# Kernel tuning notes

Measured on AMD Instinct MI355X. Metric: run time of the kernel, lower is better.

## Reference

```python
import jax, jax.numpy as jnp
import numpy as np

N_E = 1024
E_DIM = 64
BETA = 0.25


def setup_inputs() -> dict:
    key = jax.random.key(0)
    k1, k2 = jax.random.split(key)
    z = jax.random.normal(k1, (16, E_DIM, 64, 64), dtype=jnp.float32)
    # torch init: uniform(-1/n_e, 1/n_e)
    emb_w = jax.random.uniform(k2, (N_E, E_DIM), dtype=jnp.float32,
                               minval=-1.0 / N_E, maxval=1.0 / N_E)
    return {"z": z, "emb_w": emb_w}


def reference(z, emb_w):
    bt, ch, h, w = z.shape
    # (B, C, H, W) -> (B, H, W, C) -> (N, e_dim)
    z_perm = jnp.transpose(z, (0, 2, 3, 1))
    z_flat = z_perm.reshape(-1, ch)  # (N, e_dim)

    # squared euclidean distances: (N, n_e)
    distances = (jnp.sum(z_flat ** 2, axis=1, keepdims=True)
                 + jnp.sum(emb_w ** 2, axis=1)
                 - 2.0 * jnp.matmul(z_flat, emb_w.T))
    min_idx = jnp.argmin(distances, axis=1)  # (N,)

    min_encodings = jax.nn.one_hot(min_idx, N_E, dtype=z.dtype)  # (N, n_e)

    # gather codebook vectors (same math as one_hot @ emb_w)
    z_q = emb_w[min_idx].reshape(bt, h, w, ch)
    z_q = jnp.transpose(z_q, (0, 3, 1, 2))  # (B, C, H, W)

    commitment_loss = BETA * jnp.mean((jax.lax.stop_gradient(z_q) - z) ** 2)
    loss = commitment_loss

    # straight-through estimator
    z_q_st = z + jax.lax.stop_gradient(z_q - z)

    avg_probs = jnp.mean(min_encodings, axis=0)
    perplexity = jnp.exp(-jnp.sum(avg_probs * jnp.log(avg_probs + 1e-10)))

    min_encoding_indices = min_idx.reshape(bt, h, w)
    return loss, z_q_st, perplexity, min_encodings, min_encoding_indices
```

## Files before the change

### kernel.cpp

```cpp
#include <hip/hip_runtime.h>
#include <math.h>

#define NPOS   65536
#define NE     1024
#define EDIM   64
#define HW     4096
#define BETA   0.25

#define OUT_LOSS 0LL
#define OUT_ZQ   1LL
#define OUT_PERP 4194305LL
#define OUT_ENC  4194306LL
#define OUT_IDX  71303170LL

__device__ __forceinline__ float pairwise_sum_sq64(const float v[64]) {
#pragma clang fp contract(off)
    float r[8];
#pragma unroll
    for (int k = 0; k < 8; ++k) r[k] = v[k] * v[k];
#pragma unroll
    for (int i = 8; i < 64; i += 8) {
#pragma unroll
        for (int k = 0; k < 8; ++k) {
            float s = v[i + k] * v[i + k];
            r[k] = r[k] + s;
        }
    }
    return ((r[0] + r[1]) + (r[2] + r[3])) + ((r[4] + r[5]) + (r[6] + r[7]));
}

__global__ void vq_prep(const float* __restrict__ emb, float* __restrict__ enorm,
                        int* __restrict__ counts, double* __restrict__ lacc) {
    int t = blockIdx.x * 256 + threadIdx.x;
    if (t < NE) {
        float v[64];
#pragma unroll
        for (int c = 0; c < 64; ++c) v[c] = emb[t * 64 + c];
        enorm[t] = pairwise_sum_sq64(v);
        counts[t] = 0;
    }
    if (t == 0) *lacc = 0.0;
}

__global__ __launch_bounds__(256, 4)
void vq_main(const float* __restrict__ z, const float* __restrict__ emb,
             const float* __restrict__ enorm, int* __restrict__ counts,
             double* __restrict__ lacc, float* __restrict__ out) {
    __shared__ float dl[256];
    __shared__ int   il[256];
    __shared__ int   fidx[64];

    const int tid = threadIdx.x;
    const int l   = tid & 63;
    const int w   = tid >> 6;
    const int n0  = blockIdx.x * 64;
    const int b   = n0 >> 12;
    const int hw0 = n0 & 4095;
    const long long zoff = (long long)b * (64LL * HW) + hw0 + l;

    float zv[64];
#pragma unroll
    for (int c = 0; c < 64; ++c) zv[c] = z[zoff + (long long)c * HW];

    const float szn = pairwise_sum_sq64(zv);

    const int jbase = __builtin_amdgcn_readfirstlane(w * 256);

    float best = 3.4e38f;
    int   bi   = jbase;
#pragma unroll 2
    for (int jj = 0; jj < 256; ++jj) {
        const int j = jbase + jj;
        const float* __restrict__ erow = emb + j * 64;
        float acc = 0.0f;
#pragma unroll
        for (int c = 0; c < 64; ++c) acc = fmaf(zv[c], erow[c], acc);
        float dj = (szn + enorm[j]) - 2.0f * acc;
        if (dj < best) { best = dj; bi = j; }
    }
    dl[tid] = best;
    il[tid] = bi;
    __syncthreads();

    if (w == 0) {
        float bd = dl[l];
        int   bx = il[l];
#pragma unroll
        for (int ww = 1; ww < 4; ++ww) {
            float dw = dl[ww * 64 + l];
            int   iw = il[ww * 64 + l];
            if (dw < bd) { bd = dw; bx = iw; }
        }
        fidx[l] = bx;
        atomicAdd(&counts[bx], 1);
        out[OUT_IDX + n0 + l] = (float)bx;
    }
    __syncthreads();

    {
        float2* __restrict__ enc = (float2*)(out + OUT_ENC);
        const int c0 = tid * 2;
        const int c1 = (tid + 256) * 2;
        for (int r = 0; r < 64; ++r) {
            const int ir = fidx[r];
            const long long rowb = (long long)(n0 + r) * 512;
            float2 v0, v1;
            v0.x = (ir == c0)     ? 1.0f : 0.0f;
            v0.y = (ir == c0 + 1) ? 1.0f : 0.0f;
            v1.x = (ir == c1)     ? 1.0f : 0.0f;
            v1.y = (ir == c1 + 1) ? 1.0f : 0.0f;
            enc[rowb + tid]       = v0;
            enc[rowb + 256 + tid] = v1;
        }
    }

    const int myidx = fidx[l];
    double acc = 0.0;
#pragma unroll
    for (int k = 0; k < 16; ++k) {
        const int c = w * 16 + k;
        const float zc = z[zoff + (long long)c * HW];
        const float ec = emb[myidx * 64 + c];
        const float t  = __fsub_rn(ec, zc);
        const float o  = __fadd_rn(zc, t);
        out[OUT_ZQ + (long long)b * (64LL * HW) + (long long)c * HW + hw0 + l] = o;
        const float s = __fmul_rn(t, t);
        acc += (double)s;
    }
#pragma unroll
    for (int off = 32; off > 0; off >>= 1) acc += __shfl_down(acc, off);
    if (l == 0) atomicAdd(lacc, acc);
}

__global__ void vq_finalize(const int* __restrict__ counts,
                            const double* __restrict__ lacc,
                            float* __restrict__ out) {
    __shared__ float red[1024];
    const int t = threadIdx.x;
    const float p = (float)counts[t] * (1.0f / 65536.0f);
    const float term = p * logf(p + 1e-10f);
    red[t] = term;
    __syncthreads();
    for (int s = 512; s > 0; s >>= 1) {
        if (t < s) red[t] += red[t + s];
        __syncthreads();
    }
    if (t == 0) {
        out[OUT_PERP] = expf(-red[0]);
        out[OUT_LOSS] = (float)(BETA * (*lacc / 4194304.0));
    }
}

extern "C" void kernel_launch(void* const* d_in, const int* in_sizes, int n_in,
                              void* d_out, int out_size, void* d_ws, size_t ws_size,
                              hipStream_t stream) {
    const float* z   = (const float*)d_in[0];
    const float* emb = (const float*)d_in[1];
    float* out = (float*)d_out;

    double* lacc  = (double*)d_ws;
    int*    cnts  = (int*)((char*)d_ws + 16);
    float*  enorm = (float*)((char*)d_ws + 16 + NE * sizeof(int));

    vq_prep<<<4, 256, 0, stream>>>(emb, enorm, cnts, lacc);
    vq_main<<<1024, 256, 0, stream>>>(z, emb, enorm, cnts, lacc, out);
    vq_finalize<<<1, 1024, 0, stream>>>(cnts, lacc, out);
}
```

Measured before the change: 215.0 us.

## Transpose codebook and compute distances in 32-code register tiles

The prep kernel now writes a transposed copy of the codebook. The main kernel computes 32 code distances at once, streaming z one channel at a time instead of holding all 64 z values in registers. This aims to cut register pressure and increase reuse of each z load across many codes, at the cost of reloading z from memory for every 32-code tile. Offsets are also narrowed to 32-bit integers.

After: 197.1 us. 8.3% less time.

```diff
diff --git a/kernel.cpp b/kernel.cpp
--- a/kernel.cpp
+++ b/kernel.cpp
@@ -30,13 +30,16 @@
 }
 
 __global__ void vq_prep(const float* __restrict__ emb, float* __restrict__ enorm,
-                        int* __restrict__ counts, double* __restrict__ lacc) {
+                        float* __restrict__ embT, int* __restrict__ counts,
+                        double* __restrict__ lacc) {
     int t = blockIdx.x * 256 + threadIdx.x;
     if (t < NE) {
         float v[64];
 #pragma unroll
         for (int c = 0; c < 64; ++c) v[c] = emb[t * 64 + c];
         enorm[t] = pairwise_sum_sq64(v);
+#pragma unroll
+        for (int c = 0; c < 64; ++c) embT[c * NE + t] = v[c];
         counts[t] = 0;
     }
     if (t == 0) *lacc = 0.0;
@@ -44,8 +47,9 @@
 
 __global__ __launch_bounds__(256, 4)
 void vq_main(const float* __restrict__ z, const float* __restrict__ emb,
-             const float* __restrict__ enorm, int* __restrict__ counts,
-             double* __restrict__ lacc, float* __restrict__ out) {
+             const float* __restrict__ embT, const float* __restrict__ enorm,
+             int* __restrict__ counts, double* __restrict__ lacc,
+             float* __restrict__ out) {
     __shared__ float dl[256];
     __shared__ int   il[256];
     __shared__ int   fidx[64];
@@ -56,27 +60,49 @@
     const int n0  = blockIdx.x * 64;
     const int b   = n0 >> 12;
     const int hw0 = n0 & 4095;
-    const long long zoff = (long long)b * (64LL * HW) + hw0 + l;
+    const int zoff = b * (64 * HW) + hw0 + l;
 
-    float zv[64];
+    float szn;
+    {
+#pragma clang fp contract(off)
+        float r[8];
 #pragma unroll
-    for (int c = 0; c < 64; ++c) zv[c] = z[zoff + (long long)c * HW];
-
-    const float szn = pairwise_sum_sq64(zv);
+        for (int k = 0; k < 8; ++k) { float x = z[zoff + k * HW]; r[k] = x * x; }
+        for (int i = 8; i < 64; i += 8) {
+#pragma unroll
+            for (int k = 0; k < 8; ++k) {
+                float x = z[zoff + (i + k) * HW];
+                float s = x * x;
+                r[k] = r[k] + s;
+            }
+        }
+        szn = ((r[0] + r[1]) + (r[2] + r[3])) + ((r[4] + r[5]) + (r[6] + r[7]));
+    }
 
     const int jbase = __builtin_amdgcn_readfirstlane(w * 256);
 
     float best = 3.4e38f;
     int   bi   = jbase;
-#pragma unroll 2
-    for (int jj = 0; jj < 256; ++jj) {
-        const int j = jbase + jj;
-        const float* __restrict__ erow = emb + j * 64;
-        float acc = 0.0f;
+#pragma clang loop unroll(disable)
+    for (int t32 = 0; t32 < 8; ++t32) {
+        const int j0 = jbase + t32 * 32;
+        float acc[32];
 #pragma unroll
-        for (int c = 0; c < 64; ++c) acc = fmaf(zv[c], erow[c], acc);
-        float dj = (szn + enorm[j]) - 2.0f * acc;
-        if (dj < best) { best = dj; bi = j; }
+        for (int u = 0; u < 32; ++u) acc[u] = 0.0f;
+
+#pragma clang loop unroll_count(4)
+        for (int c = 0; c < 64; ++c) {
+            const float zc = z[zoff + c * HW];
+            const float* __restrict__ er = embT + c * NE + j0;
+#pragma unroll
+            for (int u = 0; u < 32; ++u) acc[u] = fmaf(zc, er[u], acc[u]);
+        }
+
+#pragma unroll
+        for (int u = 0; u < 32; ++u) {
+            const float dj = (szn + enorm[j0 + u]) - 2.0f * acc[u];
+            if (dj < best) { best = dj; bi = j0 + u; }
+        }
     }
     dl[tid] = best;
     il[tid] = bi;
@@ -119,7 +145,7 @@
 #pragma unroll
     for (int k = 0; k < 16; ++k) {
         const int c = w * 16 + k;
-        const float zc = z[zoff + (long long)c * HW];
+        const float zc = z[zoff + c * HW];
         const float ec = emb[myidx * 64 + c];
         const float t  = __fsub_rn(ec, zc);
         const float o  = __fadd_rn(zc, t);
@@ -161,8 +187,9 @@
     double* lacc  = (double*)d_ws;
     int*    cnts  = (int*)((char*)d_ws + 16);
     float*  enorm = (float*)((char*)d_ws + 16 + NE * sizeof(int));
+    float*  embT  = (float*)((char*)d_ws + 16 + NE * sizeof(int) + NE * sizeof(float));
 
-    vq_prep<<<4, 256, 0, stream>>>(emb, enorm, cnts, lacc);
-    vq_main<<<1024, 256, 0, stream>>>(z, emb, enorm, cnts, lacc, out);
+    vq_prep<<<4, 256, 0, stream>>>(emb, enorm, embT, cnts, lacc);
+    vq_main<<<1024, 256, 0, stream>>>(z, emb, embT, enorm, cnts, lacc, out);
     vq_finalize<<<1, 1024, 0, stream>>>(cnts, lacc, out);
 }
```
